# Optimization experiments

Hardware: AMD Instinct MI355X
Metric: run time of the kernel (lower is better)

## Reference

```python
import jax, jax.numpy as jnp
import numpy as np

B, H, W = 16, 32, 32
N = H * W
C_SEARCH, C_XCORR = 256, 64
C = C_SEARCH + C_XCORR          # phi_in_channels = gcn_in_channels
PHI_H = 64
GC_HID, GC_OUT = 128, 1
K_PTS = 48                       # keypoints per image
BN_EPS = 1e-5


def _build_coords_pair():
    # 8-neighbourhood pairs (distance^2 in {1,2}), exactly gen_8neigh_coords_pair
    idx = np.arange(N).reshape(H, W)
    ys, xs = np.meshgrid(np.arange(H), np.arange(W), indexing='ij')
    pairs8 = []
    for dy in (-1, 0, 1):
        for dx in (-1, 0, 1):
            if dy == 0 and dx == 0:
                continue
            ny, nx = ys + dy, xs + dx
            m = (ny >= 0) & (ny < H) & (nx >= 0) & (nx < W)
            pairs8.append(np.stack([idx[ys[m], xs[m]], idx[ny[m], nx[m]]], axis=1))
    pairs8 = np.concatenate(pairs8, 0)  # [7812, 2]
    # keypoint permutation pairs; keypoints on even coords -> disjoint from 8-neigh
    even = np.arange(0, H, 2)
    grid_idx = (even[:, None] * W + even[None, :]).reshape(-1)
    rng = np.random.default_rng(0)
    out = []
    for _ in range(B):
        kp = rng.choice(grid_idx, size=K_PTS, replace=False)
        a, b = np.meshgrid(kp, kp, indexing='ij')
        m = a != b
        kpairs = np.stack([a[m], b[m]], axis=1)  # K*(K-1) ordered pairs
        out.append(np.concatenate([kpairs, pairs8], 0))
    return np.stack(out, 0).astype(np.int32)  # [B, E, 2]


def setup_inputs() -> dict:
    key = jax.random.key(0)
    ks = jax.random.split(key, 10)
    u = lambda k, shape, s: jax.random.uniform(k, shape, jnp.float32, -s, s)
    inp = {
        'search_feature': jax.random.normal(ks[0], (B, C_SEARCH, H, W), jnp.float32),
        'xcorr_map': jax.random.normal(ks[1], (B, C_XCORR, H, W), jnp.float32),
        'coords_pair': jnp.asarray(_build_coords_pair()),
        # phi: Linear(C, PHI_H) + BN + ReLU, then Linear(PHI_H, 1) + Sigmoid
        'phi_w1': u(ks[2], (C, PHI_H), 1.0 / np.sqrt(C)),
        'phi_b1': u(ks[3], (PHI_H,), 1.0 / np.sqrt(C)),
        'bn_gamma': jnp.ones((PHI_H,), jnp.float32),
        'bn_beta': jnp.zeros((PHI_H,), jnp.float32),
        'phi_w2': u(ks[4], (PHI_H, 1), 1.0 / np.sqrt(PHI_H)),
        'phi_b2': u(ks[5], (1,), 1.0 / np.sqrt(PHI_H)),
        # GCN weights, torch init: uniform(-1/sqrt(out), 1/sqrt(out))
        'gc1_w': u(ks[6], (C, GC_HID), 1.0 / np.sqrt(GC_HID)),
        'gc2_w': u(ks[7], (GC_HID, GC_OUT), 1.0 / np.sqrt(GC_OUT)),
    }
    return inp


def reference(search_feature, xcorr_map, coords_pair, phi_w1, phi_b1,
              bn_gamma, bn_beta, phi_w2, phi_b2, gc1_w, gc2_w):
    # catted feature flattened: [B, C, N] (row-major h*W+w, matches torch view)
    feat = jnp.concatenate([search_feature, xcorr_map], axis=1).reshape(B, C, N)

    def per_image(f, pairs):  # f: [C, N], pairs: [E, 2]
        diff = jnp.abs(f[:, pairs[:, 0]] - f[:, pairs[:, 1]]).T  # [E, C]
        h = diff @ phi_w1 + phi_b1                                # [E, PHI_H]
        mu = jnp.mean(h, axis=0)
        var = jnp.var(h, axis=0)  # biased, as torch BN training mode
        h = (h - mu) / jnp.sqrt(var + BN_EPS) * bn_gamma + bn_beta
        h = jax.nn.relu(h)
        edge = jax.nn.sigmoid(h @ phi_w2 + phi_b2)[:, 0]          # [E]
        adj = jnp.zeros((N, N), jnp.float32).at[pairs[:, 0], pairs[:, 1]].set(edge)
        return adj

    adj = jax.vmap(per_image)(feat, coords_pair)  # [B, N, N]

    node_feat = feat.transpose(0, 2, 1)  # [B, N, C] (gcn_process_feat_xcorr=True)
    h = jax.nn.leaky_relu(jnp.einsum('bnm,bmd->bnd', adj, node_feat @ gc1_w), 0.2)
    mask = jax.nn.sigmoid(jnp.einsum('bnm,bmd->bnd', adj, h @ gc2_w))  # [B, N, 1]
    return mask[:, :, 0].reshape(B, 1, H, W)
```

## Files before the change

kernel.cpp:

```cpp
#include <hip/hip_runtime.h>
#include <hip/hip_bf16.h>

#define BB 16
#define NN 1024
#define CS 256
#define CX 64
#define CC 320
#define PH 64
#define GH 128
#define ELLW 64
#define NENG 7812
#define ROWP 324
#define RSTR 100
#define NKPH 1128

typedef __hip_bfloat16 bf16;
typedef __attribute__((ext_vector_type(8))) __bf16 bfrag;
typedef __attribute__((ext_vector_type(4))) float v4f;

__device__ __forceinline__ void tri_decode(int m, int& a, int& y) {
    float s = sqrtf((float)(9025 - 8 * m));
    int aa = (int)((95.0f - s) * 0.5f);
    if (aa > 0 && 47 * aa - (aa * (aa - 1)) / 2 > m) --aa;
    while (47 * (aa + 1) - ((aa + 1) * aa) / 2 <= m) ++aa;
    a = aa;
    y = aa + 1 + (m - (47 * aa - (aa * (aa - 1)) / 2));
}

__global__ __launch_bounds__(256) void k_prep(
    const float* __restrict__ w1, const float* __restrict__ gc1w,
    __bf16* __restrict__ whi, __bf16* __restrict__ wlo,
    __bf16* __restrict__ gwhi, __bf16* __restrict__ gwlo,
    int* __restrict__ cnt, float* __restrict__ Ssum, float* __restrict__ S2sum)
{
    int idx = blockIdx.x * 256 + threadIdx.x;
    if (idx < 10 * 4 * 64 * 8) {
        int j    = idx & 7;
        int lane = (idx >> 3) & 63;
        int nt   = (idx >> 9) & 3;
        int ks   = idx >> 11;
        int k = ks * 32 + (lane >> 4) * 8 + j;
        int n = nt * 16 + (lane & 15);
        float w = w1[k * PH + n];
        __bf16 h = (__bf16)w;
        whi[idx] = h;
        wlo[idx] = (__bf16)(w - (float)h);
    }
    if (idx < 10 * 8 * 64 * 8) {
        int j    = idx & 7;
        int lane = (idx >> 3) & 63;
        int nt   = (idx >> 9) & 7;
        int ks   = idx >> 12;
        int k = ks * 32 + (lane >> 4) * 8 + j;
        int n = nt * 16 + (lane & 15);
        float w = gc1w[k * GH + n];
        __bf16 h = (__bf16)w;
        gwhi[idx] = h;
        gwlo[idx] = (__bf16)(w - (float)h);
    }
    if (idx < BB * NN) cnt[idx] = 0;
    if (idx < BB * PH) { Ssum[idx] = 0.f; S2sum[idx] = 0.f; }
}

__global__ __launch_bounds__(256) void k_transpose(
    const float* __restrict__ search, const float* __restrict__ xcorr,
    float* __restrict__ featT)
{
    __shared__ float tile[32][33];
    int blk = blockIdx.x;
    int b   = blk % BB;
    int rem = blk / BB;
    int ct  = rem >> 5;
    int ntl = rem & 31;
    int tid = threadIdx.x;
    int cl = tid >> 5, nl = tid & 31;
    const float* sb = search + (size_t)b * CS * NN;
    const float* xb = xcorr + (size_t)b * CX * NN;
    #pragma unroll
    for (int f = 0; f < 4; ++f) {
        int c = ct * 32 + cl + f * 8;
        int n = ntl * 32 + nl;
        float v = (c < CS) ? sb[(size_t)c * NN + n] : xb[(size_t)(c - CS) * NN + n];
        tile[cl + f * 8][nl] = v;
    }
    __syncthreads();
    #pragma unroll
    for (int f = 0; f < 4; ++f) {
        int nr = cl + f * 8;
        int cc = nl;
        featT[((size_t)b * NN + ntl * 32 + nr) * CC + ct * 32 + cc] = tile[cc][nr];
    }
}

__global__ __launch_bounds__(512, 1) void k_edge(
    const float* __restrict__ featT, const int* __restrict__ pairs,
    const uint4* __restrict__ wglob, const float* __restrict__ b1,
    bf16* __restrict__ hstore, float* __restrict__ Ssum,
    float* __restrict__ S2sum, int E, int EKP, int nNG)
{
    __shared__ ushort Wsh[40960];
    __shared__ float RowsBuf[16000];
    __shared__ int kpn[48];

    int t = threadIdx.x;
    int wave = t >> 6, lane = t & 63;
    int q = lane >> 4, r = lane & 15;

    {
        uint4* dst = (uint4*)Wsh;
        #pragma unroll
        for (int k = 0; k < 10; ++k)
            dst[t + k * 512] = wglob[t + k * 512];
    }
    const bfrag* WH = (const bfrag*)Wsh;
    const bfrag* WL = (const bfrag*)(Wsh + 20480);

    float b1v[4];
    #pragma unroll
    for (int nt = 0; nt < 4; ++nt) b1v[nt] = b1[nt * 16 + r];
    float ps[4], ps2[4];
    #pragma unroll
    for (int nt = 0; nt < 4; ++nt) { ps[nt] = 0.f; ps2[nt] = 0.f; }
    int b;

    if (blockIdx.x < nNG) {
        b = blockIdx.x % BB;
        int s = blockIdx.x / BB;

        const int dyT[4] = {-1,-1,-1, 0};
        const int dxT[4] = {-1, 0, 1,-1};
        const int pfT8[8] = {0, 961, 1953, 2914, 3906, 4898, 5859, 6851};

        int d = wave >> 1;
        int p = wave & 1;
        int dy = dyT[d], dx = dxT[d];
        int y0 = dy < 0 ? 1 : 0;
        int x0 = dx < 0 ? 1 : 0;
        int x0R = dx > 0 ? 1 : 0;
        int ww = (dx == 0) ? 32 : 31;
        int pfF = pfT8[d];
        int pfR = pfT8[7 - d];
        int y = 2 * s + p;

        const float* rowI[2];
        const float* rowJ[2];
        #pragma unroll
        for (int mt = 0; mt < 2; ++mt) {
            int x  = (mt << 4) + r;
            int lr = 1 + p;
            int ni = lr * 32 + x;
            int xj = x + dx; xj = xj < 0 ? 0 : (xj > 31 ? 31 : xj);
            int nj = (lr + dy) * 32 + xj;
            rowI[mt] = &RowsBuf[ni * RSTR + q * 8];
            rowJ[mt] = &RowsBuf[nj * RSTR + q * 8];
        }

        v4f acc[2][4];
        #pragma unroll
        for (int mt = 0; mt < 2; ++mt)
            #pragma unroll
            for (int nt = 0; nt < 4; ++nt) acc[mt][nt] = (v4f)0.f;

        #pragma unroll
        for (int ph = 0; ph < 4; ++ph) {
            __syncthreads();
            const int ch0 = ph * 96;
            const int nf4 = (ph < 3) ? 24 : 8;
            for (int uu = t; uu < 96 * nf4; uu += 512) {
                int node = uu / nf4, c4 = uu - node * nf4;
                int gy = 2 * s - 1 + (node >> 5);
                if (gy >= 0) {
                    int gn = gy * 32 + (node & 31);
                    float4 v = *(const float4*)&featT[((size_t)b * NN + gn) * CC
                                                      + ch0 + c4 * 4];
                    *(float4*)&RowsBuf[node * RSTR + c4 * 4] = v;
                }
            }
            __syncthreads();

            const int ksBeg = ph * 3;
            const int ksEnd = (ph < 3) ? ksBeg + 3 : 10;
            #pragma unroll
            for (int ks = ksBeg; ks < ksEnd; ++ks) {
                int lc = ks * 32 - ch0;
                #pragma unroll
                for (int mt = 0; mt < 2; ++mt) {
                    float4 fi0 = *(const float4*)(rowI[mt] + lc);
                    float4 fi1 = *(const float4*)(rowI[mt] + lc + 4);
                    float4 fj0 = *(const float4*)(rowJ[mt] + lc);
                    float4 fj1 = *(const float4*)(rowJ[mt] + lc + 4);
                    float df[8];
                    df[0] = fabsf(fi0.x - fj0.x); df[1] = fabsf(fi0.y - fj0.y);
                    df[2] = fabsf(fi0.z - fj0.z); df[3] = fabsf(fi0.w - fj0.w);
                    df[4] = fabsf(fi1.x - fj1.x); df[5] = fabsf(fi1.y - fj1.y);
                    df[6] = fabsf(fi1.z - fj1.z); df[7] = fabsf(fi1.w - fj1.w);

                    bfrag ah, al;
                    #pragma unroll
                    for (int kk = 0; kk < 8; ++kk) {
                        __bf16 h = (__bf16)df[kk];
                        ah[kk] = h;
                        al[kk] = (__bf16)(df[kk] - (float)h);
                    }
                    #pragma unroll
                    for (int nt = 0; nt < 4; ++nt) {
                        bfrag bh = WH[((ks * 4 + nt) << 6) + lane];
                        bfrag bl = WL[((ks * 4 + nt) << 6) + lane];
                        acc[mt][nt] = __builtin_amdgcn_mfma_f32_16x16x32_bf16(
                            ah, bh, acc[mt][nt], 0, 0, 0);
                        acc[mt][nt] = __builtin_amdgcn_mfma_f32_16x16x32_bf16(
                            ah, bl, acc[mt][nt], 0, 0, 0);
                        acc[mt][nt] = __builtin_amdgcn_mfma_f32_16x16x32_bf16(
                            al, bh, acc[mt][nt], 0, 0, 0);
                    }
                }
            }
        }

        #pragma unroll
        for (int mt = 0; mt < 2; ++mt) {
            #pragma unroll
            for (int reg = 0; reg < 4; ++reg) {
                int xi = (mt << 4) + q * 4 + reg;
                int y2 = y + dy, x2 = xi + dx;
                bool valid = ((unsigned)y2 < 32u) && ((unsigned)x2 < 32u);
                if (valid) {
                    int e1 = EKP + pfF + (y - y0) * ww + (xi - x0);
                    int e2 = EKP + pfR + y2 * ww + (x2 - x0R);
                    bf16* h1 = hstore + ((size_t)b * E + e1) * PH + r;
                    bf16* h2 = hstore + ((size_t)b * E + e2) * PH + r;
                    #pragma unroll
                    for (int nt = 0; nt < 4; ++nt) {
                        float v = acc[mt][nt][reg] + b1v[nt];
                        bf16 vb = __float2bfloat16(v);
                        h1[nt * 16] = vb;
                        h2[nt * 16] = vb;
                        ps[nt] += v;
                        ps2[nt] = fmaf(v, v, ps2[nt]);
                    }
                }
            }
        }
    } else {
        int idx2 = blockIdx.x - nNG;
        b = idx2 % BB;
        int e0h = (idx2 / BB) * 128;
        if (t < 48) kpn[t] = pairs[((size_t)b * E + t * 47) * 2];
        __syncthreads();

        {
            const float4* src = (const float4*)featT;
            #pragma unroll
            for (int k = 0; k < 8; ++k) {
                int idx = t + k * 512;
                if (idx < 48 * 80) {
                    int slot = idx / 80, c4 = idx - slot * 80;
                    float4 v = src[((size_t)b * NN + kpn[slot]) * 80 + c4];
                    *(float4*)&RowsBuf[slot * ROWP + c4 * 4] = v;
                }
            }
        }

        int mA = e0h + wave * 16 + r;
        if (mA >= NKPH) mA = NKPH - 1;
        int aI, yI;
        tri_decode(mA, aI, yI);
        const float* rI = &RowsBuf[aI * ROWP + q * 8];
        const float* rJ = &RowsBuf[yI * ROWP + q * 8];

        v4f acc[4];
        #pragma unroll
        for (int nt = 0; nt < 4; ++nt) acc[nt] = (v4f)0.f;

        __syncthreads();

        #pragma unroll
        for (int ks = 0; ks < 10; ++ks) {
            float4 fi0 = *(const float4*)(rI + ks * 32);
            float4 fi1 = *(const float4*)(rI + ks * 32 + 4);
            float4 fj0 = *(const float4*)(rJ + ks * 32);
            float4 fj1 = *(const float4*)(rJ + ks * 32 + 4);
            float df[8];
            df[0] = fabsf(fi0.x - fj0.x); df[1] = fabsf(fi0.y - fj0.y);
            df[2] = fabsf(fi0.z - fj0.z); df[3] = fabsf(fi0.w - fj0.w);
            df[4] = fabsf(fi1.x - fj1.x); df[5] = fabsf(fi1.y - fj1.y);
            df[6] = fabsf(fi1.z - fj1.z); df[7] = fabsf(fi1.w - fj1.w);

            bfrag ah, al;
            #pragma unroll
            for (int kk = 0; kk < 8; ++kk) {
                __bf16 h = (__bf16)df[kk];
                ah[kk] = h;
                al[kk] = (__bf16)(df[kk] - (float)h);
            }
            #pragma unroll
            for (int nt = 0; nt < 4; ++nt) {
                bfrag bh = WH[((ks * 4 + nt) << 6) + lane];
                bfrag bl = WL[((ks * 4 + nt) << 6) + lane];
                acc[nt] = __builtin_amdgcn_mfma_f32_16x16x32_bf16(ah, bh, acc[nt], 0, 0, 0);
                acc[nt] = __builtin_amdgcn_mfma_f32_16x16x32_bf16(ah, bl, acc[nt], 0, 0, 0);
                acc[nt] = __builtin_amdgcn_mfma_f32_16x16x32_bf16(al, bh, acc[nt], 0, 0, 0);
            }
        }

        #pragma unroll
        for (int reg = 0; reg < 4; ++reg) {
            int mC = e0h + wave * 16 + q * 4 + reg;
            if (mC < NKPH) {
                int a, y;
                tri_decode(mC, a, y);
                int e1 = a * 47 + y - 1;
                int e2 = y * 47 + a;
                bf16* h1 = hstore + ((size_t)b * E + e1) * PH + r;
                bf16* h2 = hstore + ((size_t)b * E + e2) * PH + r;
                #pragma unroll
                for (int nt = 0; nt < 4; ++nt) {
                    float v = acc[nt][reg] + b1v[nt];
                    bf16 vb = __float2bfloat16(v);
                    h1[nt * 16] = vb;
                    h2[nt * 16] = vb;
                    ps[nt] += v;
                    ps2[nt] = fmaf(v, v, ps2[nt]);
                }
            }
        }
    }

    __syncthreads();
    float* sS  = RowsBuf;
    float* sS2 = RowsBuf + PH;
    if (t < PH) { sS[t] = 0.f; sS2[t] = 0.f; }
    __syncthreads();
    #pragma unroll
    for (int nt = 0; nt < 4; ++nt) {
        float p1 = ps[nt]  + __shfl_xor(ps[nt], 16, 64);
        p1 += __shfl_xor(p1, 32, 64);
        float p2 = ps2[nt] + __shfl_xor(ps2[nt], 16, 64);
        p2 += __shfl_xor(p2, 32, 64);
        if (lane < 16) {
            atomicAdd(&sS[nt * 16 + r],  2.0f * p1);
            atomicAdd(&sS2[nt * 16 + r], 2.0f * p2);
        }
    }
    __syncthreads();
    if (t < PH) {
        atomicAdd(&Ssum[b * PH + t],  sS[t]);
        atomicAdd(&S2sum[b * PH + t], sS2[t]);
    }
}

__global__ __launch_bounds__(256) void k_edge_val(
    const bf16* __restrict__ hstore, const float* __restrict__ Ssum,
    const float* __restrict__ S2sum, const float* __restrict__ gamma,
    const float* __restrict__ beta, const float* __restrict__ w2,
    const float* __restrict__ b2, const int* __restrict__ pairs,
    int* __restrict__ cnt, int* __restrict__ ecol, float* __restrict__ eval_,
    int E)
{
    __shared__ float ca[PH], cb[PH];
    int b = blockIdx.x % BB;
    int e = (blockIdx.x / BB) * 256 + threadIdx.x;
    if (threadIdx.x < PH) {
        int l = threadIdx.x;
        float mu = Ssum[b * PH + l] / E;
        float var = S2sum[b * PH + l] / E - mu * mu;
        float A = rsqrtf(var + 1e-5f) * gamma[l];
        ca[l] = A;
        cb[l] = beta[l] - mu * A;
    }
    __syncthreads();
    if (e >= E) return;
    const bfrag* hp = (const bfrag*)(hstore + ((size_t)b * E + e) * PH);
    float acc = 0.f;
    #pragma unroll
    for (int l8 = 0; l8 < 8; ++l8) {
        bfrag hv = hp[l8];
        #pragma unroll
        for (int c = 0; c < 8; ++c) {
            int l = l8 * 8 + c;
            float x = fmaf((float)hv[c], ca[l], cb[l]);
            x = x > 0.f ? x : 0.f;
            acc = fmaf(x, w2[l], acc);
        }
    }
    float edge = 1.f / (1.f + __expf(-(acc + b2[0])));
    const int* cp = pairs + ((size_t)b * E + e) * 2;
    int i = cp[0], j = cp[1];
    int row = b * NN + i;
    int slot = atomicAdd(&cnt[row], 1);
    if (slot < ELLW) {
        ecol[row * ELLW + slot]  = j;
        eval_[row * ELLW + slot] = edge;
    }
}

__global__ __launch_bounds__(256, 2) void k_gc1(
    const float* __restrict__ featT, const __bf16* __restrict__ gwhi,
    const __bf16* __restrict__ gwlo, float* __restrict__ g1)
{
    __shared__ ushort WG[40960];

    int t = threadIdx.x;
    int b = blockIdx.x % BB;
    int rem = blockIdx.x / BB;
    int half = rem & 1;
    int m0 = b * NN + (rem >> 1) * 64;

    {
        uint4* dst = (uint4*)WG;
        const uint4* sh = (const uint4*)gwhi;
        const uint4* sl = (const uint4*)gwlo;
        #pragma unroll
        for (int k = 0; k < 10; ++k) {
            int u = t + k * 256;
            int chunk = u >> 6, v = u & 63;
            int ks = chunk >> 2, ntp = chunk & 3;
            int src = (ks * 8 + half * 4 + ntp) * 64 + v;
            dst[u]        = sh[src];
            dst[2560 + u] = sl[src];
        }
    }

    int wave = t >> 6, lane = t & 63;
    int q = lane >> 4, r = lane & 15;
    const float* fp = featT + (size_t)(m0 + wave * 16 + r) * CC + q * 8;

    float fa[2][8];
    auto LOADA = [&](int ks, int buf) {
        const float4* p = (const float4*)(fp + ks * 32);
        *(float4*)&fa[buf][0] = p[0];
        *(float4*)&fa[buf][4] = p[1];
    };

    v4f acc[4];
    #pragma unroll
    for (int nt = 0; nt < 4; ++nt) acc[nt] = (v4f)0.f;

    LOADA(0, 0);
    __syncthreads();

    const bfrag* WGH = (const bfrag*)WG;
    const bfrag* WGL = (const bfrag*)(WG + 20480);

    #pragma unroll
    for (int ks = 0; ks < 10; ++ks) {
        int cur = ks & 1;
        if (ks < 9) LOADA(ks + 1, cur ^ 1);
        bfrag ah, al;
        #pragma unroll
        for (int kk = 0; kk < 8; ++kk) {
            float d = fa[cur][kk];
            __bf16 h = (__bf16)d;
            ah[kk] = h;
            al[kk] = (__bf16)(d - (float)h);
        }
        #pragma unroll
        for (int nt = 0; nt < 4; ++nt) {
            bfrag bh = WGH[((ks * 4 + nt) << 6) + lane];
            bfrag bl = WGL[((ks * 4 + nt) << 6) + lane];
            acc[nt] = __builtin_amdgcn_mfma_f32_16x16x32_bf16(ah, bh, acc[nt], 0, 0, 0);
            acc[nt] = __builtin_amdgcn_mfma_f32_16x16x32_bf16(ah, bl, acc[nt], 0, 0, 0);
            acc[nt] = __builtin_amdgcn_mfma_f32_16x16x32_bf16(al, bh, acc[nt], 0, 0, 0);
        }
    }
    #pragma unroll
    for (int nt = 0; nt < 4; ++nt) {
        #pragma unroll
        for (int reg = 0; reg < 4; ++reg) {
            int m = m0 + wave * 16 + q * 4 + reg;
            g1[(size_t)m * GH + (half * 4 + nt) * 16 + r] = acc[nt][reg];
        }
    }
}

__global__ __launch_bounds__(64) void k_spmm1(
    const float* __restrict__ g1, const int* __restrict__ cnt,
    const int* __restrict__ ecol, const float* __restrict__ eval_,
    const float* __restrict__ w2g, float* __restrict__ g2)
{
    int tid = threadIdx.x;
    int b = blockIdx.x % BB;
    int node = b * NN + blockIdx.x / BB;
    float wa = w2g[2 * tid], wb = w2g[2 * tid + 1];
    int c = cnt[node];
    const int* ec = ecol + (size_t)node * ELLW;
    const float* ev = eval_ + (size_t)node * ELLW;
    const float2* g1v = (const float2*)g1;
    float aa = 0.f, ab = 0.f;
    int s = 0;
    for (; s + 4 <= c; s += 4) {
        int j0 = ec[s], j1 = ec[s + 1], j2 = ec[s + 2], j3 = ec[s + 3];
        float v0 = ev[s], v1 = ev[s + 1], v2 = ev[s + 2], v3 = ev[s + 3];
        float2 u0 = g1v[((size_t)b * NN + j0) * 64 + tid];
        float2 u1 = g1v[((size_t)b * NN + j1) * 64 + tid];
        float2 u2 = g1v[((size_t)b * NN + j2) * 64 + tid];
        float2 u3 = g1v[((size_t)b * NN + j3) * 64 + tid];
        aa = fmaf(v0, u0.x, aa); ab = fmaf(v0, u0.y, ab);
        aa = fmaf(v1, u1.x, aa); ab = fmaf(v1, u1.y, ab);
        aa = fmaf(v2, u2.x, aa); ab = fmaf(v2, u2.y, ab);
        aa = fmaf(v3, u3.x, aa); ab = fmaf(v3, u3.y, ab);
    }
    for (; s < c; ++s) {
        float2 u = g1v[((size_t)b * NN + ec[s]) * 64 + tid];
        float v = ev[s];
        aa = fmaf(v, u.x, aa); ab = fmaf(v, u.y, ab);
    }
    float h1a = aa > 0.f ? aa : 0.2f * aa;
    float h1b = ab > 0.f ? ab : 0.2f * ab;
    float p = h1a * wa + h1b * wb;
    #pragma unroll
    for (int off = 32; off >= 1; off >>= 1) p += __shfl_down(p, off, 64);
    if (tid == 0) g2[node] = p;
}

__global__ __launch_bounds__(64) void k_spmm2(
    const float* __restrict__ g2, const int* __restrict__ cnt,
    const int* __restrict__ ecol, const float* __restrict__ eval_,
    float* __restrict__ out)
{
    int b = blockIdx.x % BB;
    int node = b * NN + blockIdx.x / BB;
    int lane = threadIdx.x;
    int c = cnt[node];
    float p = 0.f;
    if (lane < c) {
        int j = ecol[(size_t)node * ELLW + lane];
        p = eval_[(size_t)node * ELLW + lane] * g2[b * NN + j];
    }
    #pragma unroll
    for (int off = 32; off >= 1; off >>= 1) p += __shfl_down(p, off, 64);
    if (lane == 0) out[node] = 1.f / (1.f + __expf(-p));
}

extern "C" void kernel_launch(void* const* d_in, const int* in_sizes, int n_in,
                              void* d_out, int out_size, void* d_ws, size_t ws_size,
                              hipStream_t stream)
{
    const float* search = (const float*)d_in[0];
    const float* xcorr  = (const float*)d_in[1];
    const int*   pairs  = (const int*)d_in[2];
    const float* w1     = (const float*)d_in[3];
    const float* b1     = (const float*)d_in[4];
    const float* gamma  = (const float*)d_in[5];
    const float* beta   = (const float*)d_in[6];
    const float* w2     = (const float*)d_in[7];
    const float* b2     = (const float*)d_in[8];
    const float* gc1w   = (const float*)d_in[9];
    const float* gc2w   = (const float*)d_in[10];
    float* out = (float*)d_out;

    int E   = in_sizes[2] / (BB * 2);
    int EKP = E - NENG;
    int nb   = (E + 255) / 256;
    int nbKP = (NKPH + 127) / 128;
    int nNG  = BB * 16;

    char* ws = (char*)d_ws;
    size_t off = 0;
    auto alloc = [&](size_t bytes) {
        size_t o = off;
        off += (bytes + 255) & ~(size_t)255;
        return o;
    };
    __bf16* whi   = (__bf16*)(ws + alloc(10 * 4 * 64 * 8 * 2));
    __bf16* wlo   = (__bf16*)(ws + alloc(10 * 4 * 64 * 8 * 2));
    __bf16* gwhi  = (__bf16*)(ws + alloc(10 * 8 * 64 * 8 * 2));
    __bf16* gwlo  = (__bf16*)(ws + alloc(10 * 8 * 64 * 8 * 2));
    float* featT  = (float*)(ws + alloc((size_t)BB * NN * CC * 4));
    bf16*  hstore = (bf16*)(ws + alloc((size_t)BB * E * PH * 2));
    float* Ssum   = (float*)(ws + alloc(BB * PH * 4));
    float* S2sum  = (float*)(ws + alloc(BB * PH * 4));
    int*   cnt    = (int*)(ws + alloc(BB * NN * 4));
    int*   ecol   = (int*)(ws + alloc((size_t)BB * NN * ELLW * 4));
    float* eval_  = (float*)(ws + alloc((size_t)BB * NN * ELLW * 4));
    float* g1     = (float*)(ws + alloc((size_t)BB * NN * GH * 4));
    float* g2     = (float*)(ws + alloc(BB * NN * 4));
    (void)ws_size; (void)n_in; (void)out_size;

    k_prep<<<dim3(160), dim3(256), 0, stream>>>(w1, gc1w, whi, wlo, gwhi, gwlo,
                                                cnt, Ssum, S2sum);
    k_transpose<<<dim3(BB * 320), dim3(256), 0, stream>>>(search, xcorr, featT);
    k_edge<<<dim3(nNG + BB * nbKP), dim3(512), 0, stream>>>(featT, pairs,
                                                            (const uint4*)whi, b1,
                                                            hstore, Ssum, S2sum,
                                                            E, EKP, nNG);
    k_edge_val<<<dim3(BB * nb), dim3(256), 0, stream>>>(hstore, Ssum, S2sum,
                                                        gamma, beta, w2, b2,
                                                        pairs, cnt, ecol, eval_, E);
    k_gc1<<<dim3(BB * 32), dim3(256), 0, stream>>>(featT, gwhi, gwlo, g1);
    k_spmm1<<<dim3(BB * NN), dim3(64), 0, stream>>>(g1, cnt, ecol, eval_, gc2w, g2);
    k_spmm2<<<dim3(BB * NN), dim3(64), 0, stream>>>(g2, cnt, ecol, eval_, out);
}
```

Before: 161.1 us.

## Fuse edge MLP and BN/edge-value pass via cooperative grid sync

Merges the edge feature GEMM and the BN-normalize/sigmoid edge-value kernel into one cooperative kernel. Accumulators stay in registers across a grid-wide sync, so the bf16 hidden-state buffer round-trip through global memory goes away. Each block now handles both its neighbour rows and a slice of the keypoint pairs. The SpMM kernels are also repacked to four nodes per 256-thread block. The kernel relies on all 256 blocks being co-resident for the grid sync, and it writes ELL entries through atomics in both directions.

```diff
diff --git a/kernel.cpp b/kernel.cpp
--- a/kernel.cpp
+++ b/kernel.cpp
@@ -1,5 +1,8 @@
 #include <hip/hip_runtime.h>
 #include <hip/hip_bf16.h>
+#include <hip/hip_cooperative_groups.h>
+
+namespace cg = cooperative_groups;
 
 #define BB 16
 #define NN 1024
@@ -9,7 +12,6 @@
 #define PH 64
 #define GH 128
 #define ELLW 64
-#define NENG 7812
 #define ROWP 324
 #define RSTR 100
 #define NKPH 1128
@@ -92,11 +94,14 @@
     }
 }
 
-__global__ __launch_bounds__(512, 1) void k_edge(
+__global__ __launch_bounds__(512, 1) void k_edge_fused(
     const float* __restrict__ featT, const int* __restrict__ pairs,
     const uint4* __restrict__ wglob, const float* __restrict__ b1,
-    bf16* __restrict__ hstore, float* __restrict__ Ssum,
-    float* __restrict__ S2sum, int E, int EKP, int nNG)
+    const float* __restrict__ gamma, const float* __restrict__ beta,
+    const float* __restrict__ w2, const float* __restrict__ b2,
+    float* __restrict__ Ssum, float* __restrict__ S2sum,
+    int* __restrict__ cnt, int* __restrict__ ecol, float* __restrict__ eval_,
+    int E)
 {
     __shared__ ushort Wsh[40960];
     __shared__ float RowsBuf[16000];
@@ -105,6 +110,10 @@
     int t = threadIdx.x;
     int wave = t >> 6, lane = t & 63;
     int q = lane >> 4, r = lane & 15;
+    int b = blockIdx.x % BB;
+    int s = blockIdx.x / BB;
+
+    if (t < 48) kpn[t] = pairs[((size_t)b * E + t * 47) * 2];
 
     {
         uint4* dst = (uint4*)Wsh;
@@ -121,158 +130,134 @@
     float ps[4], ps2[4];
     #pragma unroll
     for (int nt = 0; nt < 4; ++nt) { ps[nt] = 0.f; ps2[nt] = 0.f; }
-    int b;
-
-    if (blockIdx.x < nNG) {
-        b = blockIdx.x % BB;
-        int s = blockIdx.x / BB;
-
-        const int dyT[4] = {-1,-1,-1, 0};
-        const int dxT[4] = {-1, 0, 1,-1};
-        const int pfT8[8] = {0, 961, 1953, 2914, 3906, 4898, 5859, 6851};
-
-        int d = wave >> 1;
-        int p = wave & 1;
-        int dy = dyT[d], dx = dxT[d];
-        int y0 = dy < 0 ? 1 : 0;
-        int x0 = dx < 0 ? 1 : 0;
-        int x0R = dx > 0 ? 1 : 0;
-        int ww = (dx == 0) ? 32 : 31;
-        int pfF = pfT8[d];
-        int pfR = pfT8[7 - d];
-        int y = 2 * s + p;
-
-        const float* rowI[2];
-        const float* rowJ[2];
-        #pragma unroll
-        for (int mt = 0; mt < 2; ++mt) {
-            int x  = (mt << 4) + r;
-            int lr = 1 + p;
-            int ni = lr * 32 + x;
-            int xj = x + dx; xj = xj < 0 ? 0 : (xj > 31 ? 31 : xj);
-            int nj = (lr + dy) * 32 + xj;
-            rowI[mt] = &RowsBuf[ni * RSTR + q * 8];
-            rowJ[mt] = &RowsBuf[nj * RSTR + q * 8];
-        }
-
-        v4f acc[2][4];
-        #pragma unroll
-        for (int mt = 0; mt < 2; ++mt)
+
+    const int dyT[4] = {-1,-1,-1, 0};
+    const int dxT[4] = {-1, 0, 1,-1};
+    int d = wave >> 1;
+    int p = wave & 1;
+    int dy = dyT[d], dx = dxT[d];
+    int y = 2 * s + p;
+
+    const float* rowI[2];
+    const float* rowJ[2];
+    #pragma unroll
+    for (int mt = 0; mt < 2; ++mt) {
+        int x  = (mt << 4) + r;
+        int lr = 1 + p;
+        int ni = lr * 32 + x;
+        int xj = x + dx; xj = xj < 0 ? 0 : (xj > 31 ? 31 : xj);
+        int nj = (lr + dy) * 32 + xj;
+        rowI[mt] = &RowsBuf[ni * RSTR + q * 8];
+        rowJ[mt] = &RowsBuf[nj * RSTR + q * 8];
+    }
+
+    v4f acc[2][4];
+    #pragma unroll
+    for (int mt = 0; mt < 2; ++mt)
+        #pragma unroll
+        for (int nt = 0; nt < 4; ++nt) acc[mt][nt] = (v4f)0.f;
+
+    #pragma unroll
+    for (int ph = 0; ph < 4; ++ph) {
+        __syncthreads();
+        const int ch0 = ph * 96;
+        const int nf4 = (ph < 3) ? 24 : 8;
+        for (int uu = t; uu < 96 * nf4; uu += 512) {
+            int node = uu / nf4, c4 = uu - node * nf4;
+            int gy = 2 * s - 1 + (node >> 5);
+            if (gy >= 0) {
+                int gn = gy * 32 + (node & 31);
+                float4 v = *(const float4*)&featT[((size_t)b * NN + gn) * CC
+                                                  + ch0 + c4 * 4];
+                *(float4*)&RowsBuf[node * RSTR + c4 * 4] = v;
+            }
+        }
+        __syncthreads();
+
+        const int ksBeg = ph * 3;
+        const int ksEnd = (ph < 3) ? ksBeg + 3 : 10;
+        #pragma unroll
+        for (int ks = ksBeg; ks < ksEnd; ++ks) {
+            int lc = ks * 32 - ch0;
             #pragma unroll
-            for (int nt = 0; nt < 4; ++nt) acc[mt][nt] = (v4f)0.f;
-
-        #pragma unroll
-        for (int ph = 0; ph < 4; ++ph) {
-            __syncthreads();
-            const int ch0 = ph * 96;
-            const int nf4 = (ph < 3) ? 24 : 8;
-            for (int uu = t; uu < 96 * nf4; uu += 512) {
-                int node = uu / nf4, c4 = uu - node * nf4;
-                int gy = 2 * s - 1 + (node >> 5);
-                if (gy >= 0) {
-                    int gn = gy * 32 + (node & 31);
-                    float4 v = *(const float4*)&featT[((size_t)b * NN + gn) * CC
-                                                      + ch0 + c4 * 4];
-                    *(float4*)&RowsBuf[node * RSTR + c4 * 4] = v;
+            for (int mt = 0; mt < 2; ++mt) {
+                float4 fi0 = *(const float4*)(rowI[mt] + lc);
+                float4 fi1 = *(const float4*)(rowI[mt] + lc + 4);
+                float4 fj0 = *(const float4*)(rowJ[mt] + lc);
+                float4 fj1 = *(const float4*)(rowJ[mt] + lc + 4);
+                float df[8];
+                df[0] = fabsf(fi0.x - fj0.x); df[1] = fabsf(fi0.y - fj0.y);
+                df[2] = fabsf(fi0.z - fj0.z); df[3] = fabsf(fi0.w - fj0.w);
+                df[4] = fabsf(fi1.x - fj1.x); df[5] = fabsf(fi1.y - fj1.y);
+                df[6] = fabsf(fi1.z - fj1.z); df[7] = fabsf(fi1.w - fj1.w);
+
+                bfrag ah, al;
+                #pragma unroll
+                for (int kk = 0; kk < 8; ++kk) {
+                    __bf16 h = (__bf16)df[kk];
+                    ah[kk] = h;
+                    al[kk] = (__bf16)(df[kk] - (float)h);
                 }
-            }
-            __syncthreads();
-
-            const int ksBeg = ph * 3;
-            const int ksEnd = (ph < 3) ? ksBeg + 3 : 10;
-            #pragma unroll
-            for (int ks = ksBeg; ks < ksEnd; ++ks) {
-                int lc = ks * 32 - ch0;
                 #pragma unroll
-                for (int mt = 0; mt < 2; ++mt) {
-                    float4 fi0 = *(const float4*)(rowI[mt] + lc);
-                    float4 fi1 = *(const float4*)(rowI[mt] + lc + 4);
-                    float4 fj0 = *(const float4*)(rowJ[mt] + lc);
-                    float4 fj1 = *(const float4*)(rowJ[mt] + lc + 4);
-                    float df[8];
-                    df[0] = fabsf(fi0.x - fj0.x); df[1] = fabsf(fi0.y - fj0.y);
-                    df[2] = fabsf(fi0.z - fj0.z); df[3] = fabsf(fi0.w - fj0.w);
-                    df[4] = fabsf(fi1.x - fj1.x); df[5] = fabsf(fi1.y - fj1.y);
-                    df[6] = fabsf(fi1.z - fj1.z); df[7] = fabsf(fi1.w - fj1.w);
-
-                    bfrag ah, al;
-                    #pragma unroll
-                    for (int kk = 0; kk < 8; ++kk) {
-                        __bf16 h = (__bf16)df[kk];
-                        ah[kk] = h;
-                        al[kk] = (__bf16)(df[kk] - (float)h);
-                    }
-                    #pragma unroll
-                    for (int nt = 0; nt < 4; ++nt) {
-                        bfrag bh = WH[((ks * 4 + nt) << 6) + lane];
-                        bfrag bl = WL[((ks * 4 + nt) << 6) + lane];
-                        acc[mt][nt] = __builtin_amdgcn_mfma_f32_16x16x32_bf16(
-                            ah, bh, acc[mt][nt], 0, 0, 0);
-                        acc[mt][nt] = __builtin_amdgcn_mfma_f32_16x16x32_bf16(
-                            ah, bl, acc[mt][nt], 0, 0, 0);
-                        acc[mt][nt] = __builtin_amdgcn_mfma_f32_16x16x32_bf16(
-                            al, bh, acc[mt][nt], 0, 0, 0);
-                    }
+                for (int nt = 0; nt < 4; ++nt) {
+                    bfrag bh = WH[((ks * 4 + nt) << 6) + lane];
+                    bfrag bl = WL[((ks * 4 + nt) << 6) + lane];
+                    acc[mt][nt] = __builtin_amdgcn_mfma_f32_16x16x32_bf16(
+                        ah, bh, acc[mt][nt], 0, 0, 0);
+                    acc[mt][nt] = __builtin_amdgcn_mfma_f32_16x16x32_bf16(
+                        ah, bl, acc[mt][nt], 0, 0, 0);
+                    acc[mt][nt] = __builtin_amdgcn_mfma_f32_16x16x32_bf16(
+                        al, bh, acc[mt][nt], 0, 0, 0);
                 }
             }
         }
-
-        #pragma unroll
-        for (int mt = 0; mt < 2; ++mt) {
-            #pragma unroll
-            for (int reg = 0; reg < 4; ++reg) {
-                int xi = (mt << 4) + q * 4 + reg;
-                int y2 = y + dy, x2 = xi + dx;
-                bool valid = ((unsigned)y2 < 32u) && ((unsigned)x2 < 32u);
-                if (valid) {
-                    int e1 = EKP + pfF + (y - y0) * ww + (xi - x0);
-                    int e2 = EKP + pfR + y2 * ww + (x2 - x0R);
-                    bf16* h1 = hstore + ((size_t)b * E + e1) * PH + r;
-                    bf16* h2 = hstore + ((size_t)b * E + e2) * PH + r;
-                    #pragma unroll
-                    for (int nt = 0; nt < 4; ++nt) {
-                        float v = acc[mt][nt][reg] + b1v[nt];
-                        bf16 vb = __float2bfloat16(v);
-                        h1[nt * 16] = vb;
-                        h2[nt * 16] = vb;
-                        ps[nt] += v;
-                        ps2[nt] = fmaf(v, v, ps2[nt]);
-                    }
+    }
+
+    #pragma unroll
+    for (int mt = 0; mt < 2; ++mt) {
+        #pragma unroll
+        for (int reg = 0; reg < 4; ++reg) {
+            int xi = (mt << 4) + q * 4 + reg;
+            int y2 = y + dy, x2 = xi + dx;
+            bool valid = ((unsigned)y2 < 32u) && ((unsigned)x2 < 32u);
+            if (valid) {
+                #pragma unroll
+                for (int nt = 0; nt < 4; ++nt) {
+                    float v = acc[mt][nt][reg] + b1v[nt];
+                    ps[nt] += v;
+                    ps2[nt] = fmaf(v, v, ps2[nt]);
                 }
             }
         }
-    } else {
-        int idx2 = blockIdx.x - nNG;
-        b = idx2 % BB;
-        int e0h = (idx2 / BB) * 128;
-        if (t < 48) kpn[t] = pairs[((size_t)b * E + t * 47) * 2];
-        __syncthreads();
-
-        {
-            const float4* src = (const float4*)featT;
-            #pragma unroll
-            for (int k = 0; k < 8; ++k) {
-                int idx = t + k * 512;
-                if (idx < 48 * 80) {
-                    int slot = idx / 80, c4 = idx - slot * 80;
-                    float4 v = src[((size_t)b * NN + kpn[slot]) * 80 + c4];
-                    *(float4*)&RowsBuf[slot * ROWP + c4 * 4] = v;
-                }
-            }
-        }
-
-        int mA = e0h + wave * 16 + r;
+    }
+
+    __syncthreads();
+    {
+        const float4* src = (const float4*)featT;
+        #pragma unroll
+        for (int k = 0; k < 8; ++k) {
+            int idx = t + k * 512;
+            if (idx < 48 * 80) {
+                int slot = idx / 80, c4 = idx - slot * 80;
+                float4 v = src[((size_t)b * NN + kpn[slot]) * 80 + c4];
+                *(float4*)&RowsBuf[slot * ROWP + c4 * 4] = v;
+            }
+        }
+    }
+    __syncthreads();
+
+    int u = s + 16 * wave;
+    v4f acc2[4];
+    #pragma unroll
+    for (int nt = 0; nt < 4; ++nt) acc2[nt] = (v4f)0.f;
+
+    if (u < 71) {
+        int mA = u * 16 + r;
         if (mA >= NKPH) mA = NKPH - 1;
         int aI, yI;
         tri_decode(mA, aI, yI);
         const float* rI = &RowsBuf[aI * ROWP + q * 8];
         const float* rJ = &RowsBuf[yI * ROWP + q * 8];
-
-        v4f acc[4];
-        #pragma unroll
-        for (int nt = 0; nt < 4; ++nt) acc[nt] = (v4f)0.f;
-
-        __syncthreads();
 
         #pragma unroll
         for (int ks = 0; ks < 10; ++ks) {
@@ -297,28 +282,19 @@
             for (int nt = 0; nt < 4; ++nt) {
                 bfrag bh = WH[((ks * 4 + nt) << 6) + lane];
                 bfrag bl = WL[((ks * 4 + nt) << 6) + lane];
-                acc[nt] = __builtin_amdgcn_mfma_f32_16x16x32_bf16(ah, bh, acc[nt], 0, 0, 0);
-                acc[nt] = __builtin_amdgcn_mfma_f32_16x16x32_bf16(ah, bl, acc[nt], 0, 0, 0);
-                acc[nt] = __builtin_amdgcn_mfma_f32_16x16x32_bf16(al, bh, acc[nt], 0, 0, 0);
+                acc2[nt] = __builtin_amdgcn_mfma_f32_16x16x32_bf16(ah, bh, acc2[nt], 0, 0, 0);
+                acc2[nt] = __builtin_amdgcn_mfma_f32_16x16x32_bf16(ah, bl, acc2[nt], 0, 0, 0);
+                acc2[nt] = __builtin_amdgcn_mfma_f32_16x16x32_bf16(al, bh, acc2[nt], 0, 0, 0);
             }
         }
 
         #pragma unroll
         for (int reg = 0; reg < 4; ++reg) {
-            int mC = e0h + wave * 16 + q * 4 + reg;
+            int mC = u * 16 + q * 4 + reg;
             if (mC < NKPH) {
-                int a, y;
-                tri_decode(mC, a, y);
-                int e1 = a * 47 + y - 1;
-                int e2 = y * 47 + a;
-                bf16* h1 = hstore + ((size_t)b * E + e1) * PH + r;
-                bf16* h2 = hstore + ((size_t)b * E + e2) * PH + r;
                 #pragma unroll
                 for (int nt = 0; nt < 4; ++nt) {
-                    float v = acc[nt][reg] + b1v[nt];
-                    bf16 vb = __float2bfloat16(v);
-                    h1[nt * 16] = vb;
-                    h2[nt * 16] = vb;
+                    float v = acc2[nt][reg] + b1v[nt];
                     ps[nt] += v;
                     ps2[nt] = fmaf(v, v, ps2[nt]);
                 }
@@ -347,50 +323,99 @@
         atomicAdd(&Ssum[b * PH + t],  sS[t]);
         atomicAdd(&S2sum[b * PH + t], sS2[t]);
     }
-}
-
-__global__ __launch_bounds__(256) void k_edge_val(
-    const bf16* __restrict__ hstore, const float* __restrict__ Ssum,
-    const float* __restrict__ S2sum, const float* __restrict__ gamma,
-    const float* __restrict__ beta, const float* __restrict__ w2,
-    const float* __restrict__ b2, const int* __restrict__ pairs,
-    int* __restrict__ cnt, int* __restrict__ ecol, float* __restrict__ eval_,
-    int E)
-{
-    __shared__ float ca[PH], cb[PH];
-    int b = blockIdx.x % BB;
-    int e = (blockIdx.x / BB) * 256 + threadIdx.x;
-    if (threadIdx.x < PH) {
-        int l = threadIdx.x;
-        float mu = Ssum[b * PH + l] / E;
-        float var = S2sum[b * PH + l] / E - mu * mu;
-        float A = rsqrtf(var + 1e-5f) * gamma[l];
-        ca[l] = A;
-        cb[l] = beta[l] - mu * A;
-    }
-    __syncthreads();
-    if (e >= E) return;
-    const bfrag* hp = (const bfrag*)(hstore + ((size_t)b * E + e) * PH);
-    float acc = 0.f;
-    #pragma unroll
-    for (int l8 = 0; l8 < 8; ++l8) {
-        bfrag hv = hp[l8];
-        #pragma unroll
-        for (int c = 0; c < 8; ++c) {
-            int l = l8 * 8 + c;
-            float x = fmaf((float)hv[c], ca[l], cb[l]);
-            x = x > 0.f ? x : 0.f;
-            acc = fmaf(x, w2[l], acc);
-        }
-    }
-    float edge = 1.f / (1.f + __expf(-(acc + b2[0])));
-    const int* cp = pairs + ((size_t)b * E + e) * 2;
-    int i = cp[0], j = cp[1];
-    int row = b * NN + i;
-    int slot = atomicAdd(&cnt[row], 1);
-    if (slot < ELLW) {
-        ecol[row * ELLW + slot]  = j;
-        eval_[row * ELLW + slot] = edge;
+
+    __threadfence();
+    cg::this_grid().sync();
+
+    float Einv = 1.0f / (float)E;
+    float An[4], Cb[4], Wv[4];
+    #pragma unroll
+    for (int nt = 0; nt < 4; ++nt) {
+        int l = nt * 16 + r;
+        float Sv  = __hip_atomic_load(&Ssum[b * PH + l],
+                                      __ATOMIC_RELAXED, __HIP_MEMORY_SCOPE_AGENT);
+        float S2v = __hip_atomic_load(&S2sum[b * PH + l],
+                                      __ATOMIC_RELAXED, __HIP_MEMORY_SCOPE_AGENT);
+        float mu  = Sv * Einv;
+        float var = S2v * Einv - mu * mu;
+        float Aa  = rsqrtf(var + 1e-5f) * gamma[l];
+        An[nt] = Aa;
+        Cb[nt] = beta[l] - mu * Aa;
+        Wv[nt] = w2[l];
+    }
+    float b2v = b2[0];
+
+    {
+        float selP = 0.f;
+        int selI = 0, selJ = 0, selV = 0;
+        #pragma unroll
+        for (int mt = 0; mt < 2; ++mt) {
+            #pragma unroll
+            for (int reg = 0; reg < 4; ++reg) {
+                float pp = 0.f;
+                #pragma unroll
+                for (int nt = 0; nt < 4; ++nt) {
+                    float v = acc[mt][nt][reg] + b1v[nt];
+                    float x = fmaf(v, An[nt], Cb[nt]);
+                    x = x > 0.f ? x : 0.f;
+                    pp = fmaf(x, Wv[nt], pp);
+                }
+                pp += __shfl_xor(pp, 1, 64);
+                pp += __shfl_xor(pp, 2, 64);
+                pp += __shfl_xor(pp, 4, 64);
+                pp += __shfl_xor(pp, 8, 64);
+                int idx = mt * 4 + reg;
+                int xi = (mt << 4) + q * 4 + reg;
+                int y2 = y + dy, x2 = xi + dx;
+                int vld = (((unsigned)y2 < 32u) && ((unsigned)x2 < 32u)) ? 1 : 0;
+                if (r == idx) {
+                    selP = pp; selI = y * 32 + xi; selJ = y2 * 32 + x2; selV = vld;
+                }
+            }
+        }
+        if (selV) {
+            float ev2 = 1.f / (1.f + __expf(-(selP + b2v)));
+            int ri = b * NN + selI;
+            int rj = b * NN + selJ;
+            int s1 = atomicAdd(&cnt[ri], 1);
+            if (s1 < ELLW) { ecol[ri * ELLW + s1] = selJ; eval_[ri * ELLW + s1] = ev2; }
+            int s2 = atomicAdd(&cnt[rj], 1);
+            if (s2 < ELLW) { ecol[rj * ELLW + s2] = selI; eval_[rj * ELLW + s2] = ev2; }
+        }
+    }
+
+    if (u < 71) {
+        float selP = 0.f;
+        int selM = -1;
+        #pragma unroll
+        for (int reg = 0; reg < 4; ++reg) {
+            float pp = 0.f;
+            #pragma unroll
+            for (int nt = 0; nt < 4; ++nt) {
+                float v = acc2[nt][reg] + b1v[nt];
+                float x = fmaf(v, An[nt], Cb[nt]);
+                x = x > 0.f ? x : 0.f;
+                pp = fmaf(x, Wv[nt], pp);
+            }
+            pp += __shfl_xor(pp, 1, 64);
+            pp += __shfl_xor(pp, 2, 64);
+            pp += __shfl_xor(pp, 4, 64);
+            pp += __shfl_xor(pp, 8, 64);
+            int mC = u * 16 + q * 4 + reg;
+            if (r == reg && mC < NKPH) { selP = pp; selM = mC; }
+        }
+        if (selM >= 0) {
+            float ev2 = 1.f / (1.f + __expf(-(selP + b2v)));
+            int a2, y2k;
+            tri_decode(selM, a2, y2k);
+            int i = kpn[a2], j = kpn[y2k];
+            int ri = b * NN + i;
+            int rj = b * NN + j;
+            int s1 = atomicAdd(&cnt[ri], 1);
+            if (s1 < ELLW) { ecol[ri * ELLW + s1] = j; eval_[ri * ELLW + s1] = ev2; }
+            int s2 = atomicAdd(&cnt[rj], 1);
+            if (s2 < ELLW) { ecol[rj * ELLW + s2] = i; eval_[rj * ELLW + s2] = ev2; }
+        }
     }
 }
 
@@ -473,14 +498,14 @@
     }
 }
 
-__global__ __launch_bounds__(64) void k_spmm1(
+__global__ __launch_bounds__(256) void k_spmm1(
     const float* __restrict__ g1, const int* __restrict__ cnt,
     const int* __restrict__ ecol, const float* __restrict__ eval_,
     const float* __restrict__ w2g, float* __restrict__ g2)
 {
-    int tid = threadIdx.x;
-    int b = blockIdx.x % BB;
-    int node = b * NN + blockIdx.x / BB;
+    int tid = threadIdx.x & 63;
+    int node = blockIdx.x * 4 + (threadIdx.x >> 6);
+    int base = node & ~(NN - 1);
     float wa = w2g[2 * tid], wb = w2g[2 * tid + 1];
     int c = cnt[node];
     const int* ec = ecol + (size_t)node * ELLW;
@@ -491,17 +516,17 @@
     for (; s + 4 <= c; s += 4) {
         int j0 = ec[s], j1 = ec[s + 1], j2 = ec[s + 2], j3 = ec[s + 3];
         float v0 = ev[s], v1 = ev[s + 1], v2 = ev[s + 2], v3 = ev[s + 3];
-        float2 u0 = g1v[((size_t)b * NN + j0) * 64 + tid];
-        float2 u1 = g1v[((size_t)b * NN + j1) * 64 + tid];
-        float2 u2 = g1v[((size_t)b * NN + j2) * 64 + tid];
-        float2 u3 = g1v[((size_t)b * NN + j3) * 64 + tid];
+        float2 u0 = g1v[((size_t)(base + j0)) * 64 + tid];
+        float2 u1 = g1v[((size_t)(base + j1)) * 64 + tid];
+        float2 u2 = g1v[((size_t)(base + j2)) * 64 + tid];
+        float2 u3 = g1v[((size_t)(base + j3)) * 64 + tid];
         aa = fmaf(v0, u0.x, aa); ab = fmaf(v0, u0.y, ab);
         aa = fmaf(v1, u1.x, aa); ab = fmaf(v1, u1.y, ab);
         aa = fmaf(v2, u2.x, aa); ab = fmaf(v2, u2.y, ab);
         aa = fmaf(v3, u3.x, aa); ab = fmaf(v3, u3.y, ab);
     }
     for (; s < c; ++s) {
-        float2 u = g1v[((size_t)b * NN + ec[s]) * 64 + tid];
+        float2 u = g1v[((size_t)(base + ec[s])) * 64 + tid];
         float v = ev[s];
         aa = fmaf(v, u.x, aa); ab = fmaf(v, u.y, ab);
     }
@@ -513,19 +538,19 @@
     if (tid == 0) g2[node] = p;
 }
 
-__global__ __launch_bounds__(64) void k_spmm2(
+__global__ __launch_bounds__(256) void k_spmm2(
     const float* __restrict__ g2, const int* __restrict__ cnt,
     const int* __restrict__ ecol, const float* __restrict__ eval_,
     float* __restrict__ out)
 {
-    int b = blockIdx.x % BB;
-    int node = b * NN + blockIdx.x / BB;
-    int lane = threadIdx.x;
+    int lane = threadIdx.x & 63;
+    int node = blockIdx.x * 4 + (threadIdx.x >> 6);
+    int base = node & ~(NN - 1);
     int c = cnt[node];
     float p = 0.f;
     if (lane < c) {
         int j = ecol[(size_t)node * ELLW + lane];
-        p = eval_[(size_t)node * ELLW + lane] * g2[b * NN + j];
+        p = eval_[(size_t)node * ELLW + lane] * g2[base + j];
     }
     #pragma unroll
     for (int off = 32; off >= 1; off >>= 1) p += __shfl_down(p, off, 64);
@@ -549,11 +574,7 @@
     const float* gc2w   = (const float*)d_in[10];
     float* out = (float*)d_out;
 
-    int E   = in_sizes[2] / (BB * 2);
-    int EKP = E - NENG;
-    int nb   = (E + 255) / 256;
-    int nbKP = (NKPH + 127) / 128;
-    int nNG  = BB * 16;
+    int E = in_sizes[2] / (BB * 2);
 
     char* ws = (char*)d_ws;
     size_t off = 0;
@@ -567,7 +588,6 @@
     __bf16* gwhi  = (__bf16*)(ws + alloc(10 * 8 * 64 * 8 * 2));
     __bf16* gwlo  = (__bf16*)(ws + alloc(10 * 8 * 64 * 8 * 2));
     float* featT  = (float*)(ws + alloc((size_t)BB * NN * CC * 4));
-    bf16*  hstore = (bf16*)(ws + alloc((size_t)BB * E * PH * 2));
     float* Ssum   = (float*)(ws + alloc(BB * PH * 4));
     float* S2sum  = (float*)(ws + alloc(BB * PH * 4));
     int*   cnt    = (int*)(ws + alloc(BB * NN * 4));
@@ -580,14 +600,19 @@
     k_prep<<<dim3(160), dim3(256), 0, stream>>>(w1, gc1w, whi, wlo, gwhi, gwlo,
                                                 cnt, Ssum, S2sum);
     k_transpose<<<dim3(BB * 320), dim3(256), 0, stream>>>(search, xcorr, featT);
-    k_edge<<<dim3(nNG + BB * nbKP), dim3(512), 0, stream>>>(featT, pairs,
-                                                            (const uint4*)whi, b1,
-                                                            hstore, Ssum, S2sum,
-                                                            E, EKP, nNG);
-    k_edge_val<<<dim3(BB * nb), dim3(256), 0, stream>>>(hstore, Ssum, S2sum,
-                                                        gamma, beta, w2, b2,
-                                                        pairs, cnt, ecol, eval_, E);
     k_gc1<<<dim3(BB * 32), dim3(256), 0, stream>>>(featT, gwhi, gwlo, g1);
-    k_spmm1<<<dim3(BB * NN), dim3(64), 0, stream>>>(g1, cnt, ecol, eval_, gc2w, g2);
-    k_spmm2<<<dim3(BB * NN), dim3(64), 0, stream>>>(g2, cnt, ecol, eval_, out);
-}
+
+    const uint4* wglob = (const uint4*)whi;
+    void* cargs[] = {
+        (void*)&featT, (void*)&pairs, (void*)&wglob, (void*)&b1,
+        (void*)&gamma, (void*)&beta, (void*)&w2, (void*)&b2,
+        (void*)&Ssum, (void*)&S2sum, (void*)&cnt, (void*)&ecol,
+        (void*)&eval_, (void*)&E
+    };
+    hipLaunchCooperativeKernel(k_edge_fused, dim3(BB * 16), dim3(512),
+                               cargs, 0, stream);
+
+    k_spmm1<<<dim3(BB * NN / 4), dim3(256), 0, stream>>>(g1, cnt, ecol, eval_,
+                                                         gc2w, g2);
+    k_spmm2<<<dim3(BB * NN / 4), dim3(256), 0, stream>>>(g2, cnt, ecol, eval_, out);
+}
```

Result: slower. 229.8 us (+42.7%).
